# Optimization experiments

Hardware: AMD Instinct MI355X
Metric: run time of the kernel (lower is better)

## Reference

```python
import jax, jax.numpy as jnp
import numpy as np

N_NODES = 100000
N_EDGES = 3200000
H, D = 3, 12  # heads, per-head dim; H*D == node_hidden_dim == 36
NEG_SLOPE = 0.2


def setup_inputs() -> dict:
    key = jax.random.key(0)
    ks = jax.random.split(key, 11)
    s = 0.1
    return {
        "node_features": jax.random.normal(ks[0], (N_NODES, 36), jnp.float32),
        "src": jax.random.randint(ks[1], (N_EDGES,), 0, N_NODES),
        "dst": jax.random.randint(ks[2], (N_EDGES,), 0, N_NODES),
        "lin0_w": jax.random.normal(ks[3], (36, 36), jnp.float32) * s,
        "lin0_b": jax.random.normal(ks[4], (36,), jnp.float32) * s,
        "fc_w": jax.random.normal(ks[5], (3, 36, 36), jnp.float32) * s,
        "attn_l": jax.random.normal(ks[6], (3, H, D), jnp.float32) * s,
        "attn_r": jax.random.normal(ks[7], (3, H, D), jnp.float32) * s,
        "gat_bias": jax.random.normal(ks[8], (3, 36), jnp.float32) * s,
        "out_w": jax.random.normal(ks[9], (36, 36), jnp.float32) * s,
        "out_b": jax.random.normal(ks[10], (36,), jnp.float32) * s,
    }


def _gat_layer(h, src, dst, fc_w, a_l, a_r, bias):
    n = h.shape[0]
    feat = (h @ fc_w).reshape(n, H, D)                      # (N,H,D)
    el = jnp.sum(feat * a_l, axis=-1)                       # (N,H)
    er = jnp.sum(feat * a_r, axis=-1)                       # (N,H)
    e = el[src] + er[dst]                                   # (E,H)
    e = jnp.where(e >= 0, e, NEG_SLOPE * e)                 # leaky_relu(0.2)
    # edge softmax over incoming edges of each dst node (numerically stable)
    m = jax.ops.segment_max(e, dst, num_segments=n)         # (N,H)
    m = jnp.where(jnp.isfinite(m), m, 0.0)                  # zero-degree guard
    ee = jnp.exp(e - m[dst])                                # (E,H)
    denom = jax.ops.segment_sum(ee, dst, num_segments=n)    # (N,H)
    alpha = ee / jnp.maximum(denom[dst], 1e-9)              # (E,H)
    msg = feat[src] * alpha[:, :, None]                     # (E,H,D)
    rst = jax.ops.segment_sum(msg, dst, num_segments=n)     # (N,H,D)
    # residual (Identity since in_feats == H*D) + bias, then ELU
    rst = rst + h.reshape(n, H, D) + bias.reshape(1, H, D)
    return jax.nn.elu(rst).reshape(n, H * D)


def reference(node_features, src, dst, lin0_w, lin0_b, fc_w, attn_l, attn_r, gat_bias, out_w, out_b):
    h = node_features @ lin0_w + lin0_b
    for l in range(3):
        h = _gat_layer(h, src, dst, fc_w[l], attn_l[l], attn_r[l], gat_bias[l])
    return h @ out_w + out_b
```

## Files before the change

### kernel.cpp

```cpp
#include <hip/hip_runtime.h>
#include <math.h>

#define HID 36
#define NH 3
#define HD 12
#define PROW 64
#define BSHIFT 13
#define NBUCK 13
#define PSHIFT 8
#define PCHUNK 2048
#define SPCAP 9216
#define CSRCAP 4096
#define NSTEP 8

typedef _Float16 f16;


__global__ void __launch_bounds__(256, 1)
lin0_hist_kernel(const float* __restrict__ x, const float* __restrict__ w0,
                 const float* __restrict__ b0, const float* __restrict__ fcw,
                 const float* __restrict__ al, const float* __restrict__ ar,
                 float* __restrict__ h, f16* __restrict__ packed,
                 float* __restrict__ er, int n, int nb_lin,
                 const int* __restrict__ dst, int* __restrict__ M, int E, int C,
                 int np) {
    int t = threadIdx.x;
    if ((int)blockIdx.x >= nb_lin) {
        __shared__ int hcnt[512];
        int c = blockIdx.x - nb_lin;
        for (int i = t; i < 512; i += 256) hcnt[i] = 0;
        __syncthreads();
        int i0 = c * PCHUNK;
        int i1 = min(i0 + PCHUNK, E);
        for (int i = i0 + t; i < i1; i += 256)
            atomicAdd(&hcnt[dst[i] >> PSHIFT], 1);
        __syncthreads();
        for (int b = t; b < np; b += 256)
            M[(size_t)b * C + c] = hcnt[b];
        return;
    }
    __shared__ float W0[HID * HID];
    __shared__ float W1[HID * HID];
    __shared__ float Bs[HID], ALs[HID], ARs[HID];
    for (int i = t; i < HID * HID; i += 256) { W0[i] = w0[i]; W1[i] = fcw[i]; }
    if (t < HID) { Bs[t] = b0[t]; ALs[t] = al[t]; ARs[t] = ar[t]; }
    __syncthreads();
    int node = blockIdx.x * 256 + t;
    if (node >= n) return;
    const float4* xp = (const float4*)(x + (size_t)node * HID);
    float h0[HID];
#pragma unroll
    for (int j = 0; j < HID; ++j) h0[j] = Bs[j];
#pragma unroll
    for (int kk = 0; kk < HID / 4; ++kk) {
        float4 xv = xp[kk];
        const float* w = &W0[(4 * kk) * HID];
#pragma unroll
        for (int j = 0; j < HID; ++j)
            h0[j] += xv.x * w[j] + xv.y * w[HID + j] + xv.z * w[2 * HID + j] + xv.w * w[3 * HID + j];
    }
    float* hp = h + (size_t)node * HID;
#pragma unroll
    for (int j = 0; j < HID; ++j) hp[j] = h0[j];
    float feat[HID];
#pragma unroll
    for (int j = 0; j < HID; ++j) feat[j] = 0.f;
#pragma unroll
    for (int k = 0; k < HID; ++k) {
        float hv = h0[k];
        const float* w = &W1[k * HID];
#pragma unroll
        for (int j = 0; j < HID; ++j) feat[j] += hv * w[j];
    }
    union { f16 hx[48]; uint4 q[6]; } u;
#pragma unroll
    for (int hh = 0; hh < NH; ++hh) {
        float sl = 0.f, sr = 0.f;
#pragma unroll
        for (int d = 0; d < HD; ++d) {
            sl += feat[hh * HD + d] * ALs[hh * HD + d];
            sr += feat[hh * HD + d] * ARs[hh * HD + d];
        }
#pragma unroll
        for (int d = 0; d < HD; ++d) u.hx[hh * 16 + d] = (f16)feat[hh * HD + d];
        u.hx[hh * 16 + 12] = (f16)sl;
        u.hx[hh * 16 + 13] = (f16)0.f;
        u.hx[hh * 16 + 14] = (f16)0.f;
        u.hx[hh * 16 + 15] = (f16)0.f;
        er[node * NH + hh] = sr;
    }
    uint4* prow = (uint4*)(packed + (size_t)node * PROW);
#pragma unroll
    for (int q = 0; q < 6; ++q) prow[q] = u.q[q];
}

__global__ void base_scan_kernel(const int* __restrict__ M, int* __restrict__ BaseT,
                                 int* __restrict__ T, int C, int np) {
    __shared__ int tmp[512];
    int b = blockIdx.x;
    int t = threadIdx.x;
    int carry = 0;
    for (int base = 0; base < C; base += 512) {
        int idx = base + t;
        int v = (idx < C) ? M[(size_t)b * C + idx] : 0;
        tmp[t] = v;
        __syncthreads();
        for (int ofs = 1; ofs < 512; ofs <<= 1) {
            int x = 0;
            if (t >= ofs) x = tmp[t - ofs];
            __syncthreads();
            tmp[t] += x;
            __syncthreads();
        }
        if (idx < C) BaseT[(size_t)idx * 512 + b] = carry + tmp[t] - v;
        carry += tmp[511];
        __syncthreads();
    }
    if (t == 0) T[b] = carry;
}

__global__ void part_scatter_kernel(const int* __restrict__ src, const int* __restrict__ dst,
                                    const int* __restrict__ BaseT, const int* __restrict__ T,
                                    int* __restrict__ part, int E, int np) {
    __shared__ int tsc[512];
    __shared__ int base[512];
    __shared__ int hexcl[512];
    __shared__ int hcur[512];
    __shared__ int smsrc[PCHUNK];
    __shared__ int smdst[PCHUNK];
    __shared__ int smsort[PCHUNK];
    __shared__ short smbin[PCHUNK];
    int t = threadIdx.x;
    int c = blockIdx.x;
    int v = (t < np) ? T[t] : 0;
    tsc[t] = v;
    hcur[t] = 0;
    __syncthreads();
    for (int ofs = 1; ofs < 512; ofs <<= 1) {
        int x = 0;
        if (t >= ofs) x = tsc[t - ofs];
        __syncthreads();
        tsc[t] += x;
        __syncthreads();
    }
    if (t < np) base[t] = (tsc[t] - v) + BaseT[(size_t)c * 512 + t];
    __syncthreads();
    int i0 = c * PCHUNK;
    int cnum = min(i0 + PCHUNK, E) - i0;
    for (int i = t; i < cnum; i += 512) {
        int s = src[i0 + i], d = dst[i0 + i];
        smsrc[i] = s;
        smdst[i] = d;
        atomicAdd(&hcur[d >> PSHIFT], 1);
    }
    __syncthreads();
    int hv = hcur[t];
    tsc[t] = hv;
    __syncthreads();
    for (int ofs = 1; ofs < 512; ofs <<= 1) {
        int x = 0;
        if (t >= ofs) x = tsc[t - ofs];
        __syncthreads();
        tsc[t] += x;
        __syncthreads();
    }
    hexcl[t] = tsc[t] - hv;
    hcur[t] = tsc[t] - hv;
    __syncthreads();
    for (int i = t; i < cnum; i += 512) {
        int d = smdst[i];
        int bin = d >> PSHIFT;
        int pos = atomicAdd(&hcur[bin], 1);
        smsort[pos] = (smsrc[i] << PSHIFT) | (d & ((1 << PSHIFT) - 1));
        smbin[pos] = (short)bin;
    }
    __syncthreads();
    for (int i = t; i < cnum; i += 512) {
        int bin = smbin[i];
        part[base[bin] + (i - hexcl[bin])] = smsort[i];
    }
}

__global__ void bucket_csr_kernel(const int* __restrict__ part, const int* __restrict__ T,
                                  int* __restrict__ csr, int* __restrict__ off,
                                  int n, int E, int np) {
    __shared__ int cnt[256 * NBUCK];
    __shared__ int psum[512];
    __shared__ int smout[SPCAP];
    __shared__ int e0s;
    int p = blockIdx.x;
    int t = threadIdx.x;
    int v = (t < np) ? T[t] : 0;
    psum[t] = v;
    __syncthreads();
    for (int ofs = 1; ofs < 512; ofs <<= 1) {
        int x = 0;
        if (t >= ofs) x = psum[t - ofs];
        __syncthreads();
        psum[t] += x;
        __syncthreads();
    }
    if (t == p) e0s = psum[t] - v;
    __syncthreads();
    int e0 = e0s;
    int dbase = p << PSHIFT;
    int nd = min(256, n - dbase);
    int nc = nd * NBUCK;
    for (int i = t; i < nc; i += blockDim.x) cnt[i] = 0;
    __syncthreads();
    int cnt_p = T[p];
    const int* pp = part + e0;
    bool fits = (cnt_p <= SPCAP);
    for (int i = t; i < cnt_p; i += blockDim.x) {
        int e = pp[i];
        atomicAdd(&cnt[(e & 255) * NBUCK + ((e >> PSHIFT) >> BSHIFT)], 1);
    }
    __syncthreads();
    int sum = 0;
    if (t < nd) {
        for (int k = 0; k < NBUCK; ++k) {
            int c = cnt[t * NBUCK + k];
            cnt[t * NBUCK + k] = sum;
            sum += c;
        }
    }
    psum[t] = (t < nd) ? sum : 0;
    __syncthreads();
    for (int ofs = 1; ofs < 512; ofs <<= 1) {
        int x = 0;
        if (t >= ofs) x = psum[t - ofs];
        __syncthreads();
        psum[t] += x;
        __syncthreads();
    }
    int dexcl = (t > 0) ? psum[t - 1] : 0;
    int start = e0 + dexcl;
    if (t < nd) {
        for (int k = 0; k < NBUCK; ++k) cnt[t * NBUCK + k] += start;
        off[dbase + t] = start;
    }
    __syncthreads();
    if (fits) {
        for (int i = t; i < cnt_p; i += blockDim.x) {
            int e = pp[i];
            int s = e >> PSHIFT;
            int idx = (e & 255) * NBUCK + (s >> BSHIFT);
            int pos = atomicAdd(&cnt[idx], 1);
            smout[pos - e0] = s << 6;
        }
        __syncthreads();
        for (int i = t; i < cnt_p; i += blockDim.x)
            csr[e0 + i] = smout[i];
    } else {
        for (int i = t; i < cnt_p; i += blockDim.x) {
            int e = pp[i];
            int s = e >> PSHIFT;
            int idx = (e & 255) * NBUCK + (s >> BSHIFT);
            int pos = atomicAdd(&cnt[idx], 1);
            csr[pos] = s << 6;
        }
    }
    if (p == 0 && t == 0) off[n] = E;
}


__device__ __forceinline__ void edge_accum(uint4 qa, uint4 qb, float ern,
                                           float& denom, float* acc) {
    union { uint4 q[2]; f16 hx[16]; } v;
    v.q[0] = qa;
    v.q[1] = qb;
    float e = (float)v.hx[12] + ern;
    e = (e >= 0.f) ? e : 0.2f * e;
    float w = __expf(e);
    denom += w;
#pragma unroll
    for (int k = 0; k < HD; ++k) acc[k] += w * (float)v.hx[k];
}

template <bool FITS>
__device__ __forceinline__ void sweep_paced(const int* __restrict__ smbuf,
                                            const int* __restrict__ csre,
                                            int j0, int deg, const f16* __restrict__ pb,
                                            float ern, float& denom, float* acc) {
    int j = j0;
#pragma unroll 1
    for (int s2 = 1; s2 <= NSTEP; ++s2) {
        int jend = j0 + ((deg * s2) >> 3);
        int c = jend - j;
        for (; c >= 4; c -= 4, j += 4) {
            int o0 = FITS ? smbuf[j]     : csre[j];
            int o1 = FITS ? smbuf[j + 1] : csre[j + 1];
            int o2 = FITS ? smbuf[j + 2] : csre[j + 2];
            int o3 = FITS ? smbuf[j + 3] : csre[j + 3];
            const uint4* r0 = (const uint4*)(pb + o0);
            const uint4* r1 = (const uint4*)(pb + o1);
            const uint4* r2 = (const uint4*)(pb + o2);
            const uint4* r3 = (const uint4*)(pb + o3);
            uint4 a0 = r0[0], b0 = r0[1];
            uint4 a1 = r1[0], b1 = r1[1];
            uint4 a2 = r2[0], b2 = r2[1];
            uint4 a3 = r3[0], b3 = r3[1];
            edge_accum(a0, b0, ern, denom, acc);
            edge_accum(a1, b1, ern, denom, acc);
            edge_accum(a2, b2, ern, denom, acc);
            edge_accum(a3, b3, ern, denom, acc);
        }
        for (; c > 0; --c, ++j) {
            int o = FITS ? smbuf[j] : csre[j];
            const uint4* r = (const uint4*)(pb + o);
            edge_accum(r[0], r[1], ern, denom, acc);
        }
    }
}

__global__ void __launch_bounds__(192)
aggtr_kernel(const f16* __restrict__ packed_in, const float* __restrict__ er_in,
             const float* __restrict__ hcur,
             const int* __restrict__ off, const int* __restrict__ csr,
             const float* __restrict__ bias, const float* __restrict__ wnext,
             const float* __restrict__ aln, const float* __restrict__ arn,
             float* __restrict__ hnext, f16* __restrict__ packed_out,
             float* __restrict__ er_out, int n) {
    __shared__ float Wsh[HID * HID];
    __shared__ float ALs[HID], ARs[HID];
    __shared__ int smbuf[CSRCAP];
    int t = threadIdx.x;
    for (int i = t; i < HID * HID; i += 192) Wsh[i] = wnext[i];
    if (t < HID) { ALs[t] = aln[t]; ARs[t] = arn[t]; }
    int ln = t / 3, hh = t - ln * 3;
    int nb0 = blockIdx.x * 64;
    int node = nb0 + ln;
    bool active = (node < n);

    int e0 = off[nb0];
    int e1 = off[min(nb0 + 64, n)];
    int span = e1 - e0;
    bool fits = (span <= CSRCAP);
    if (fits)
        for (int i = t; i < span; i += 192) smbuf[i] = csr[e0 + i];

    int j0 = 0, deg = 0;
    float ern = 0.f;
    if (active) {
        j0 = off[node] - e0;
        deg = off[node + 1] - e0 - j0;
        ern = er_in[node * NH + hh];
    }
    const f16* pb = packed_in + hh * 16;
    const int* csre = csr + e0;
    __syncthreads();

    float denom = 0.f;
    float acc[HD];
#pragma unroll
    for (int k = 0; k < HD; ++k) acc[k] = 0.f;

    if (fits) sweep_paced<true>(smbuf, csre, j0, deg, pb, ern, denom, acc);
    else      sweep_paced<false>(smbuf, csre, j0, deg, pb, ern, denom, acc);
    __syncthreads();

    float* hsh = (float*)smbuf;
    float v[HD];
#pragma unroll
    for (int k = 0; k < HD; ++k) v[k] = 0.f;
    if (active) {
        float inv = 1.f / fmaxf(denom, 1e-9f);
        int base = node * HID + hh * HD;
        const float4* hc = (const float4*)(hcur + base);
        float4 h0 = hc[0], h1 = hc[1], h2 = hc[2];
        float hres[HD] = {h0.x, h0.y, h0.z, h0.w, h1.x, h1.y, h1.z, h1.w, h2.x, h2.y, h2.z, h2.w};
#pragma unroll
        for (int k = 0; k < HD; ++k) {
            float x = acc[k] * inv + hres[k] + bias[hh * HD + k];
            v[k] = (x > 0.f) ? x : expm1f(x);
        }
        float4* hp = (float4*)(hnext + base);
        hp[0] = make_float4(v[0], v[1], v[2], v[3]);
        hp[1] = make_float4(v[4], v[5], v[6], v[7]);
        hp[2] = make_float4(v[8], v[9], v[10], v[11]);
    }
#pragma unroll
    for (int k = 0; k < HD; ++k) hsh[ln * 37 + hh * HD + k] = v[k];
    __syncthreads();

    float feat[HD];
#pragma unroll
    for (int d = 0; d < HD; ++d) feat[d] = 0.f;
    const float* hrow = &hsh[ln * 37];
#pragma unroll 4
    for (int k = 0; k < HID; ++k) {
        float hv = hrow[k];
        const float* w = &Wsh[k * HID + hh * HD];
#pragma unroll
        for (int d = 0; d < HD; ++d) feat[d] += hv * w[d];
    }
    if (!active) return;
    float sl = 0.f, sr = 0.f;
#pragma unroll
    for (int d = 0; d < HD; ++d) {
        sl += feat[d] * ALs[hh * HD + d];
        sr += feat[d] * ARs[hh * HD + d];
    }
    union { f16 hx[16]; uint4 q[2]; } o;
#pragma unroll
    for (int d = 0; d < HD; ++d) o.hx[d] = (f16)feat[d];
    o.hx[12] = (f16)sl;
    o.hx[13] = (f16)0.f; o.hx[14] = (f16)0.f; o.hx[15] = (f16)0.f;
    uint4* prow = (uint4*)(packed_out + (size_t)node * PROW + hh * 16);
    prow[0] = o.q[0];
    prow[1] = o.q[1];
    er_out[node * NH + hh] = sr;
}

__global__ void __launch_bounds__(192)
aggout_kernel(const f16* __restrict__ packed_in, const float* __restrict__ er_in,
              const float* __restrict__ hcur,
              const int* __restrict__ off, const int* __restrict__ csr,
              const float* __restrict__ bias, const float* __restrict__ ow,
              const float* __restrict__ ob, float* __restrict__ out, int n) {
    __shared__ float Wsh[HID * HID];
    __shared__ float OBs[HID];
    __shared__ int smbuf[CSRCAP];
    int t = threadIdx.x;
    for (int i = t; i < HID * HID; i += 192) Wsh[i] = ow[i];
    if (t < HID) OBs[t] = ob[t];
    int ln = t / 3, hh = t - ln * 3;
    int nb0 = blockIdx.x * 64;
    int node = nb0 + ln;
    bool active = (node < n);

    int e0 = off[nb0];
    int e1 = off[min(nb0 + 64, n)];
    int span = e1 - e0;
    bool fits = (span <= CSRCAP);
    if (fits)
        for (int i = t; i < span; i += 192) smbuf[i] = csr[e0 + i];

    int j0 = 0, deg = 0;
    float ern = 0.f;
    if (active) {
        j0 = off[node] - e0;
        deg = off[node + 1] - e0 - j0;
        ern = er_in[node * NH + hh];
    }
    const f16* pb = packed_in + hh * 16;
    const int* csre = csr + e0;
    __syncthreads();

    float denom = 0.f;
    float acc[HD];
#pragma unroll
    for (int k = 0; k < HD; ++k) acc[k] = 0.f;

    if (fits) sweep_paced<true>(smbuf, csre, j0, deg, pb, ern, denom, acc);
    else      sweep_paced<false>(smbuf, csre, j0, deg, pb, ern, denom, acc);
    __syncthreads();

    float* hsh = (float*)smbuf;
    float v[HD];
#pragma unroll
    for (int k = 0; k < HD; ++k) v[k] = 0.f;
    if (active) {
        float inv = 1.f / fmaxf(denom, 1e-9f);
        int base = node * HID + hh * HD;
        const float4* hc = (const float4*)(hcur + base);
        float4 h0 = hc[0], h1 = hc[1], h2 = hc[2];
        float hres[HD] = {h0.x, h0.y, h0.z, h0.w, h1.x, h1.y, h1.z, h1.w, h2.x, h2.y, h2.z, h2.w};
#pragma unroll
        for (int k = 0; k < HD; ++k) {
            float x = acc[k] * inv + hres[k] + bias[hh * HD + k];
            v[k] = (x > 0.f) ? x : expm1f(x);
        }
    }
#pragma unroll
    for (int k = 0; k < HD; ++k) hsh[ln * 37 + hh * HD + k] = v[k];
    __syncthreads();

    float feat[HD];
#pragma unroll
    for (int d = 0; d < HD; ++d) feat[d] = OBs[hh * HD + d];
    const float* hrow = &hsh[ln * 37];
#pragma unroll 4
    for (int k = 0; k < HID; ++k) {
        float hv = hrow[k];
        const float* w = &Wsh[k * HID + hh * HD];
#pragma unroll
        for (int d = 0; d < HD; ++d) feat[d] += hv * w[d];
    }
    if (!active) return;
    float4* op = (float4*)(out + (size_t)node * HID + hh * HD);
    op[0] = make_float4(feat[0], feat[1], feat[2], feat[3]);
    op[1] = make_float4(feat[4], feat[5], feat[6], feat[7]);
    op[2] = make_float4(feat[8], feat[9], feat[10], feat[11]);
}


extern "C" void kernel_launch(void* const* d_in, const int* in_sizes, int n_in,
                              void* d_out, int out_size, void* d_ws, size_t ws_size,
                              hipStream_t stream) {
    const float* xnf = (const float*)d_in[0];
    const int* src = (const int*)d_in[1];
    const int* dst = (const int*)d_in[2];
    const float* l0w = (const float*)d_in[3];
    const float* l0b = (const float*)d_in[4];
    const float* fcw = (const float*)d_in[5];
    const float* al  = (const float*)d_in[6];
    const float* ar  = (const float*)d_in[7];
    const float* gb  = (const float*)d_in[8];
    const float* ow  = (const float*)d_in[9];
    const float* ob  = (const float*)d_in[10];
    float* out = (float*)d_out;
    const int N = in_sizes[0] / HID;
    const int E = in_sizes[1];
    const int NP = (N + (1 << PSHIFT) - 1) >> PSHIFT;
    const int C = (E + PCHUNK - 1) / PCHUNK;

    char* p = (char*)d_ws;
    auto alloc = [&](size_t bytes) {
        char* r = p;
        p += (bytes + 255) & ~(size_t)255;
        return r;
    };
    int* part    = (int*)alloc((size_t)E * 4);
    int* M       = (int*)alloc((size_t)NP * C * 4);
    int* BaseT   = (int*)alloc((size_t)C * 512 * 4);
    int* T       = (int*)alloc((size_t)NP * 4);
    int* off     = (int*)alloc((size_t)(N + 1) * 4);
    int* csr     = (int*)alloc((size_t)E * 4);
    float* ha    = (float*)alloc((size_t)N * HID * 4);
    float* hb    = (float*)alloc((size_t)N * HID * 4);
    f16* pkA     = (f16*)alloc((size_t)N * PROW * 2);
    f16* pkB     = (f16*)alloc((size_t)N * PROW * 2);
    float* erA   = (float*)alloc((size_t)N * NH * 4);
    float* erB   = (float*)alloc((size_t)N * NH * 4);

    int nblk = (N + 255) / 256;
    int fblk = (N + 63) / 64;

    lin0_hist_kernel<<<nblk + C, 256, 0, stream>>>(xnf, l0w, l0b, fcw, al, ar,
                                                   ha, pkA, erA, N, nblk,
                                                   dst, M, E, C, NP);
    base_scan_kernel<<<NP, 512, 0, stream>>>(M, BaseT, T, C, NP);
    part_scatter_kernel<<<C, 512, 0, stream>>>(src, dst, BaseT, T, part, E, NP);
    bucket_csr_kernel<<<NP, 512, 0, stream>>>(part, T, csr, off, N, E, NP);

    aggtr_kernel<<<fblk, 192, 0, stream>>>(pkA, erA, ha, off, csr, gb,
                                           fcw + (size_t)1 * HID * HID, al + HID, ar + HID,
                                           hb, pkB, erB, N);
    aggtr_kernel<<<fblk, 192, 0, stream>>>(pkB, erB, hb, off, csr, gb + HID,
                                           fcw + (size_t)2 * HID * HID, al + 2 * HID, ar + 2 * HID,
                                           ha, pkA, erA, N);
    aggout_kernel<<<fblk, 192, 0, stream>>>(pkA, erA, ha, off, csr, gb + 2 * HID,
                                            ow, ob, out, N);
}
```

Before: 337.4 us.

## Split lin0 node transform across three threads per node with LDS-staged input

The fused lin0 + first-layer projection kernel now assigns three threads per node, one per head, so each thread computes only 12 output features instead of 36. Input rows are staged through padded shared memory with coalesced loads, and the lin0 output is shared via LDS for the second matmul. The launch moves to 192-thread blocks covering 64 nodes, and the launch_bounds min-blocks hint is dropped. The aim is to cut per-thread register pressure and improve memory coalescing, at the cost of extra LDS traffic and a block-wide sync; the histogram branch simply adapts its strides.

```diff
diff --git a/kernel.cpp b/kernel.cpp
--- a/kernel.cpp
+++ b/kernel.cpp
@@ -16,7 +16,7 @@
 typedef _Float16 f16;
 
 
-__global__ void __launch_bounds__(256, 1)
+__global__ void __launch_bounds__(192)
 lin0_hist_kernel(const float* __restrict__ x, const float* __restrict__ w0,
                  const float* __restrict__ b0, const float* __restrict__ fcw,
                  const float* __restrict__ al, const float* __restrict__ ar,
@@ -28,70 +28,84 @@
     if ((int)blockIdx.x >= nb_lin) {
         __shared__ int hcnt[512];
         int c = blockIdx.x - nb_lin;
-        for (int i = t; i < 512; i += 256) hcnt[i] = 0;
+        for (int i = t; i < 512; i += 192) hcnt[i] = 0;
         __syncthreads();
         int i0 = c * PCHUNK;
         int i1 = min(i0 + PCHUNK, E);
-        for (int i = i0 + t; i < i1; i += 256)
+        for (int i = i0 + t; i < i1; i += 192)
             atomicAdd(&hcnt[dst[i] >> PSHIFT], 1);
         __syncthreads();
-        for (int b = t; b < np; b += 256)
+        for (int b = t; b < np; b += 192)
             M[(size_t)b * C + c] = hcnt[b];
         return;
     }
     __shared__ float W0[HID * HID];
     __shared__ float W1[HID * HID];
     __shared__ float Bs[HID], ALs[HID], ARs[HID];
-    for (int i = t; i < HID * HID; i += 256) { W0[i] = w0[i]; W1[i] = fcw[i]; }
+    __shared__ float xsh[64 * 37];
+    __shared__ float hsh[64 * 37];
+    for (int i = t; i < HID * HID; i += 192) { W0[i] = w0[i]; W1[i] = fcw[i]; }
     if (t < HID) { Bs[t] = b0[t]; ALs[t] = al[t]; ARs[t] = ar[t]; }
-    __syncthreads();
-    int node = blockIdx.x * 256 + t;
-    if (node >= n) return;
-    const float4* xp = (const float4*)(x + (size_t)node * HID);
-    float h0[HID];
-#pragma unroll
-    for (int j = 0; j < HID; ++j) h0[j] = Bs[j];
-#pragma unroll
-    for (int kk = 0; kk < HID / 4; ++kk) {
-        float4 xv = xp[kk];
-        const float* w = &W0[(4 * kk) * HID];
-#pragma unroll
-        for (int j = 0; j < HID; ++j)
-            h0[j] += xv.x * w[j] + xv.y * w[HID + j] + xv.z * w[2 * HID + j] + xv.w * w[3 * HID + j];
-    }
-    float* hp = h + (size_t)node * HID;
-#pragma unroll
-    for (int j = 0; j < HID; ++j) hp[j] = h0[j];
-    float feat[HID];
-#pragma unroll
-    for (int j = 0; j < HID; ++j) feat[j] = 0.f;
-#pragma unroll
+    int nb0 = blockIdx.x * 64;
+    int nrow = min(64, n - nb0);
+    for (int i = t; i < nrow * HID; i += 192) {
+        int r = i / HID, cc = i - r * HID;
+        xsh[r * 37 + cc] = x[(size_t)nb0 * HID + i];
+        (void)cc;
+    }
+    __syncthreads();
+    int ln = t / 3, hh = t - ln * 3;
+    int node = nb0 + ln;
+    bool active = (node < n);
+
+    float h0s[HD];
+#pragma unroll
+    for (int d = 0; d < HD; ++d) h0s[d] = Bs[hh * HD + d];
+    const float* xrow = &xsh[ln * 37];
+#pragma unroll 4
     for (int k = 0; k < HID; ++k) {
-        float hv = h0[k];
-        const float* w = &W1[k * HID];
-#pragma unroll
-        for (int j = 0; j < HID; ++j) feat[j] += hv * w[j];
-    }
-    union { f16 hx[48]; uint4 q[6]; } u;
-#pragma unroll
-    for (int hh = 0; hh < NH; ++hh) {
-        float sl = 0.f, sr = 0.f;
-#pragma unroll
-        for (int d = 0; d < HD; ++d) {
-            sl += feat[hh * HD + d] * ALs[hh * HD + d];
-            sr += feat[hh * HD + d] * ARs[hh * HD + d];
-        }
-#pragma unroll
-        for (int d = 0; d < HD; ++d) u.hx[hh * 16 + d] = (f16)feat[hh * HD + d];
-        u.hx[hh * 16 + 12] = (f16)sl;
-        u.hx[hh * 16 + 13] = (f16)0.f;
-        u.hx[hh * 16 + 14] = (f16)0.f;
-        u.hx[hh * 16 + 15] = (f16)0.f;
-        er[node * NH + hh] = sr;
-    }
-    uint4* prow = (uint4*)(packed + (size_t)node * PROW);
-#pragma unroll
-    for (int q = 0; q < 6; ++q) prow[q] = u.q[q];
+        float xv = xrow[k];
+        const float* w = &W0[k * HID + hh * HD];
+#pragma unroll
+        for (int d = 0; d < HD; ++d) h0s[d] += xv * w[d];
+    }
+    if (active) {
+        float4* hp = (float4*)(h + (size_t)node * HID + hh * HD);
+        hp[0] = make_float4(h0s[0], h0s[1], h0s[2], h0s[3]);
+        hp[1] = make_float4(h0s[4], h0s[5], h0s[6], h0s[7]);
+        hp[2] = make_float4(h0s[8], h0s[9], h0s[10], h0s[11]);
+    }
+#pragma unroll
+    for (int d = 0; d < HD; ++d) hsh[ln * 37 + hh * HD + d] = h0s[d];
+    __syncthreads();
+
+    float feat[HD];
+#pragma unroll
+    for (int d = 0; d < HD; ++d) feat[d] = 0.f;
+    const float* hrow = &hsh[ln * 37];
+#pragma unroll 4
+    for (int k = 0; k < HID; ++k) {
+        float hv = hrow[k];
+        const float* w = &W1[k * HID + hh * HD];
+#pragma unroll
+        for (int d = 0; d < HD; ++d) feat[d] += hv * w[d];
+    }
+    if (!active) return;
+    float sl = 0.f, sr = 0.f;
+#pragma unroll
+    for (int d = 0; d < HD; ++d) {
+        sl += feat[d] * ALs[hh * HD + d];
+        sr += feat[d] * ARs[hh * HD + d];
+    }
+    union { f16 hx[16]; uint4 q[2]; } o;
+#pragma unroll
+    for (int d = 0; d < HD; ++d) o.hx[d] = (f16)feat[d];
+    o.hx[12] = (f16)sl;
+    o.hx[13] = (f16)0.f; o.hx[14] = (f16)0.f; o.hx[15] = (f16)0.f;
+    uint4* prow = (uint4*)(packed + (size_t)node * PROW + hh * 16);
+    prow[0] = o.q[0];
+    prow[1] = o.q[1];
+    er[node * NH + hh] = sr;
 }
 
 __global__ void base_scan_kernel(const int* __restrict__ M, int* __restrict__ BaseT,
@@ -534,12 +548,12 @@
     float* erA   = (float*)alloc((size_t)N * NH * 4);
     float* erB   = (float*)alloc((size_t)N * NH * 4);
 
-    int nblk = (N + 255) / 256;
+    int nblk_lin = (N + 63) / 64;
     int fblk = (N + 63) / 64;
 
-    lin0_hist_kernel<<<nblk + C, 256, 0, stream>>>(xnf, l0w, l0b, fcw, al, ar,
-                                                   ha, pkA, erA, N, nblk,
-                                                   dst, M, E, C, NP);
+    lin0_hist_kernel<<<nblk_lin + C, 192, 0, stream>>>(xnf, l0w, l0b, fcw, al, ar,
+                                                       ha, pkA, erA, N, nblk_lin,
+                                                       dst, M, E, C, NP);
     base_scan_kernel<<<NP, 512, 0, stream>>>(M, BaseT, T, C, NP);
     part_scatter_kernel<<<C, 512, 0, stream>>>(src, dst, BaseT, T, part, E, NP);
     bucket_csr_kernel<<<NP, 512, 0, stream>>>(part, T, csr, off, N, E, NP);
```

After: 336.6 us. About the same (-0.2%).
